# Kernel tuning notes

Hardware: AMD Instinct MI355X
Metric: run time of the kernel (lower is better)

Reference implementation:

```python
import jax, jax.numpy as jnp
import numpy as np

# --- Cl(3,0,1) projective geometric algebra structure constants (GATr blade order) ---
BLADES = [(), (0,), (1,), (2,), (3,), (0, 1), (0, 2), (0, 3), (1, 2), (1, 3), (2, 3),
          (0, 1, 2), (0, 1, 3), (0, 2, 3), (1, 2, 3), (0, 1, 2, 3)]
IDX = {b: i for i, b in enumerate(BLADES)}
METRIC = [0.0, 1.0, 1.0, 1.0]  # e0 degenerate, e1,e2,e3 square to +1


def _mul_blades(a, b):
    """Multiply two basis blades; returns (sign, sorted_blade_tuple)."""
    lst = list(a) + list(b)
    sign = 1.0
    changed = True
    while changed:
        changed = False
        k = 0
        while k < len(lst) - 1:
            if lst[k] > lst[k + 1]:
                lst[k], lst[k + 1] = lst[k + 1], lst[k]
                sign = -sign
                changed = True
            elif lst[k] == lst[k + 1]:
                sign *= METRIC[lst[k]]
                del lst[k:k + 2]
                changed = True
            else:
                k += 1
    return sign, tuple(lst)


def _tables():
    gp = np.zeros((16, 16, 16), np.float32)
    outer = np.zeros((16, 16, 16), np.float32)
    for j, bj in enumerate(BLADES):
        for k, bk in enumerate(BLADES):
            s, bl = _mul_blades(bj, bk)
            if s != 0.0:
                gp[IDX[bl], j, k] = s
            if set(bj).isdisjoint(bk):  # outer product: nonzero only for disjoint blades
                outer[IDX[bl], j, k] = s
    # dual map D: blade -> signed complement, with blade ^ complement = sign * e0123
    D = np.zeros((16, 16), np.float32)
    for j, bj in enumerate(BLADES):
        comp = tuple(i for i in range(4) if i not in bj)
        s, _ = _mul_blades(bj, comp)
        D[IDX[comp], j] = s
    # join(x, y) = dual(dual(x) ^ dual(y))  ->  bilinear tensor [16,16,16]
    join = np.einsum('ai,ijk,jb,kc->abc', D, outer, D, D).astype(np.float32)
    # Pin-equivariant linear basis: 5 grade projections + 4 e0-wedge-per-grade maps
    grades = np.array([len(b) for b in BLADES])
    basis = np.zeros((9, 16, 16), np.float32)
    for g in range(5):
        basis[g] = np.diag((grades == g).astype(np.float32))
    e0_mul = outer[:, IDX[(0,)], :]  # x -> e0 ^ x
    for g in range(4):
        basis[5 + g] = e0_mul * (grades == g)[None, :].astype(np.float32)
    return gp, join, basis


B, N = 8, 4096
IN_MV, HID, OUT_MV = 32, 32, 32
HALF = HID // 2
IN_S, OUT_S = 64, 64
NB = 9


def setup_inputs() -> dict:
    key = jax.random.key(0)
    ks = jax.random.split(key, 16)
    gp, jn, basis = _tables()

    def wmv(k, o, i):
        return jax.random.normal(k, (o, i, NB), jnp.float32) / np.sqrt(i * NB)

    def ws(k, o, i):
        return jax.random.normal(k, (o, i), jnp.float32) / np.sqrt(i)

    return dict(
        multivectors=jax.random.normal(ks[0], (B, N, IN_MV, 16), jnp.float32),
        reference_mv=jax.random.normal(ks[1], (B, N, 16), jnp.float32),
        scalars=jax.random.normal(ks[2], (B, N, IN_S), jnp.float32),
        basis=jnp.asarray(basis), gp=jnp.asarray(gp), jn=jnp.asarray(jn),
        w_left_mv=wmv(ks[3], HALF, IN_MV), w_left_s=ws(ks[4], HALF, IN_S),
        w_right_mv=wmv(ks[5], HALF, IN_MV), w_right_s=ws(ks[6], HALF, IN_S),
        w_jl_mv=wmv(ks[7], HALF, IN_MV), w_jl_s=ws(ks[8], HALF, IN_S),
        w_jr_mv=wmv(ks[9], HALF, IN_MV), w_jr_s=ws(ks[10], HALF, IN_S),
        w_out_mv=wmv(ks[11], OUT_MV, HID), w_out_s2mv=ws(ks[12], OUT_MV, IN_S),
        w_out_mvs2s=ws(ks[13], OUT_S, HID), w_out_s2s=ws(ks[14], OUT_S, IN_S),
    )


def _equi_linear(x, s, w_mv, w_s, basis):
    # fold the 9 equivariant basis maps into the channel-mixing weight once (tiny)
    W = jnp.einsum('oib,bjk->oijk', w_mv, basis)  # [out, in, 16, 16]
    out = jnp.einsum('oijk,...ik->...oj', W, x)   # (..., out, 16)
    # scalar inputs feed the multivector scalar component (blade index 0)
    out = out.at[..., 0].add(jnp.einsum('os,...s->...o', w_s, s))
    return out


def reference(multivectors, reference_mv, scalars, basis, gp, jn,
              w_left_mv, w_left_s, w_right_mv, w_right_s, w_jl_mv, w_jl_s,
              w_jr_mv, w_jr_s, w_out_mv, w_out_s2mv, w_out_mvs2s, w_out_s2s):
    left = _equi_linear(multivectors, scalars, w_left_mv, w_left_s, basis)
    right = _equi_linear(multivectors, scalars, w_right_mv, w_right_s, basis)
    gp_out = jnp.einsum('ijk,...cj,...ck->...ci', gp, left, right)  # geometric product

    jl = _equi_linear(multivectors, scalars, w_jl_mv, w_jl_s, basis)
    jr = _equi_linear(multivectors, scalars, w_jr_mv, w_jr_s, basis)
    # equivariant join, scaled by pseudoscalar (e0123) component of the reference
    join_out = jnp.einsum('ijk,...cj,...ck->...ci', jn, jl, jr) * reference_mv[..., None, 15:16]

    hidden = jnp.concatenate([gp_out, join_out], axis=-2)  # (..., HID, 16)
    out_mv = _equi_linear(hidden, scalars, w_out_mv, w_out_s2mv, basis)
    out_s = jnp.einsum('oc,...c->...o', w_out_mvs2s, hidden[..., 0]) \
        + jnp.einsum('os,...s->...o', w_out_s2s, scalars)
    return out_mv, out_s
```

## Files before the change

kernel.cpp:

```cpp
#include <hip/hip_runtime.h>
#include <stdint.h>


#define NPOS_TOTAL 32768

typedef __attribute__((ext_vector_type(8))) short short8;
typedef __attribute__((ext_vector_type(4))) float f32x4;
#define MFMA16(a,b,c) __builtin_amdgcn_mfma_f32_16x16x32_bf16((a),(b),(c),0,0,0)

constexpr int BLADE_MASK[16] = {0,1,2,4,8,3,5,9,6,10,12,7,11,13,14,15};
constexpr int MASK2IDX[16]   = {0,1,2,5,3,6,8,11,4,7,9,12,10,13,14,15};

struct MulRes { int sign; int mask; };

constexpr MulRes mul_blades(int ma, int mb) {
  int lst[8] = {0,0,0,0,0,0,0,0};
  int n = 0;
  for (int g = 0; g < 4; ++g) if ((ma >> g) & 1) lst[n++] = g;
  for (int g = 0; g < 4; ++g) if ((mb >> g) & 1) lst[n++] = g;
  int sign = 1;
  bool changed = true;
  while (changed) {
    changed = false;
    int k = 0;
    while (k + 1 < n) {
      if (lst[k] > lst[k+1]) {
        int t = lst[k]; lst[k] = lst[k+1]; lst[k+1] = t;
        sign = -sign; changed = true;
      } else if (lst[k] == lst[k+1]) {
        if (lst[k] == 0) sign = 0;
        for (int m = k; m + 2 < n; ++m) lst[m] = lst[m+2];
        n -= 2; changed = true;
      } else {
        ++k;
      }
    }
  }
  int mask = 0;
  for (int m = 0; m < n; ++m) mask |= (1 << lst[m]);
  if (sign == 0) mask = 0;
  return MulRes{sign, mask};
}

struct Tables {
  float gp_sgn[16][16]; int gp_idx[16][16];
  float jn_sgn[16][16]; int jn_idx[16][16];
  constexpr Tables() : gp_sgn{}, gp_idx{}, jn_sgn{}, jn_idx{} {
    for (int j = 0; j < 16; ++j) {
      for (int k = 0; k < 16; ++k) {
        MulRes r = mul_blades(BLADE_MASK[j], BLADE_MASK[k]);
        gp_sgn[j][k] = (float)r.sign;
        gp_idx[j][k] = MASK2IDX[r.mask & 15];
        jn_sgn[j][k] = 0.0f; jn_idx[j][k] = 0;
        int mb = BLADE_MASK[j], mc = BLADE_MASK[k];
        if ((mb | mc) == 15) {
          int cb = 15 ^ mb, cc = 15 ^ mc;
          MulRes sb = mul_blades(mb, cb);
          MulRes sc = mul_blades(mc, cc);
          MulRes ro = mul_blades(cb, cc);
          int imask = ro.mask;
          int amask = 15 ^ imask;
          MulRes si = mul_blades(imask, amask);
          jn_sgn[j][k] = (float)(si.sign * ro.sign * sb.sign * sc.sign);
          jn_idx[j][k] = MASK2IDX[amask & 15];
        }
      }
    }
  }
};
constexpr Tables TBL{};

constexpr int GRADE[16] = {0,1,1,1,1,2,2,2,2,2,2,3,3,3,3,4};
constexpr int E0_TGT[8]  = {1,5,6,7,11,12,13,15};
constexpr int E0_SRC[8]  = {0,2,3,4,8,9,10,14};
constexpr int E0_SLOT[8] = {5,6,6,6,7,7,7,8};

__device__ __forceinline__ float bflo(unsigned u) { return __uint_as_float(u << 16); }
__device__ __forceinline__ float bfhi(unsigned u) { return __uint_as_float(u & 0xffff0000u); }
__device__ __forceinline__ unsigned pk2(float a, float b) {
  unsigned ua = __float_as_uint(a), ub = __float_as_uint(b);
  unsigned ra = (ua + 0x7fffu + ((ua >> 16) & 1u)) >> 16;
  unsigned rb = (ub + 0x7fffu + ((ub >> 16) & 1u)) >> 16;
  return (ra & 0xffffu) | ((rb & 0xffffu) << 16);
}
__device__ __forceinline__ unsigned short bf1(float a) {
  unsigned ua = __float_as_uint(a);
  return (unsigned short)((ua + 0x7fffu + ((ua >> 16) & 1u)) >> 16);
}

__global__ void gb_prep(const float* __restrict__ wlmv, const float* __restrict__ wrmv,
                        const float* __restrict__ wjlmv, const float* __restrict__ wjrmv,
                        const float* __restrict__ wls,  const float* __restrict__ wrs,
                        const float* __restrict__ wjls, const float* __restrict__ wjrs,
                        const float* __restrict__ womv, const float* __restrict__ ws2mv,
                        const float* __restrict__ wm2s, const float* __restrict__ ws2s,
                        uint4* __restrict__ wpk) {
  int t = blockIdx.x * 256 + threadIdx.x;
  if (t >= 78 * 64) return;
  int blk = t >> 6, l = t & 63;
  int m = l & 15, q = l >> 4;
  float v[8];
  if (blk < 36) {
    int slot = blk >> 2, ot = blk & 3;
    const float* wmv[4] = {wlmv, wrmv, wjlmv, wjrmv};
    for (int jj = 0; jj < 8; ++jj) {
      int k = q * 8 + jj;
      v[jj] = wmv[ot][m * 288 + k * 9 + slot];
    }
  } else if (blk < 44) {
    int b = blk - 36, h = b >> 2, ot = b & 3;
    const float* wsc[4] = {wls, wrs, wjls, wjrs};
    for (int jj = 0; jj < 8; ++jj) {
      int k = q * 8 + jj;
      v[jj] = wsc[ot][m * 64 + h * 32 + k];
    }
  } else if (blk < 62) {
    int b = blk - 44, slot = b >> 1, ot = b & 1;
    int o = ot * 16 + m;
    for (int jj = 0; jj < 8; ++jj) {
      int k = q * 8 + jj;
      v[jj] = womv[o * 288 + k * 9 + slot];
    }
  } else if (blk < 66) {
    int b = blk - 62, h = b >> 1, ot = b & 1;
    int o = ot * 16 + m;
    for (int jj = 0; jj < 8; ++jj) {
      int k = q * 8 + jj;
      v[jj] = ws2mv[o * 64 + h * 32 + k];
    }
  } else if (blk < 70) {
    int ot = blk - 66, o = ot * 16 + m;
    for (int jj = 0; jj < 8; ++jj) {
      int k = q * 8 + jj;
      v[jj] = wm2s[o * 32 + k];
    }
  } else {
    int b = blk - 70, half = b >> 2, ot = b & 3;
    int o = ot * 16 + m;
    for (int jj = 0; jj < 8; ++jj) {
      int k = q * 8 + jj;
      v[jj] = ws2s[o * 64 + half * 32 + k];
    }
  }
  uint4 u;
  u.x = pk2(v[0], v[1]); u.y = pk2(v[2], v[3]);
  u.z = pk2(v[4], v[5]); u.w = pk2(v[6], v[7]);
  wpk[t] = u;
}

__global__ __launch_bounds__(256, 2) void gb_main(
    const float* __restrict__ mv, const float* __restrict__ ref,
    const float* __restrict__ s, const uint4* __restrict__ wpk,
    float* __restrict__ out_mv, float* __restrict__ out_s) {
  __shared__ __align__(16) char smem[54016];
  unsigned short* xs_e = (unsigned short*)smem;
  unsigned*       xs_w = (unsigned*)smem;
  unsigned short* hl_e = (unsigned short*)smem;
  unsigned*       yl_w = (unsigned*)(smem + 16640);

  const int tid  = threadIdx.x;
  const int wave = tid >> 6, lane = tid & 63;
  const int lm = lane & 15, lq = lane >> 4;
  const int P0 = blockIdx.x * 16;

  short8 wg[5];
  #pragma unroll
  for (int g = 0; g < 5; ++g)
    wg[g] = __builtin_bit_cast(short8, wpk[(g * 4 + wave) * 64 + lane]);

  const float rs = ref[((size_t)(P0 + (tid & 15))) * 16 + 15];

  const float4* mv4 = (const float4*)mv + (size_t)P0 * 128;
  #pragma unroll
  for (int kk = 0; kk < 4; ++kk) {
    int e = tid + kk * 256;
    int p = e >> 6, sub = e & 63, i2 = sub >> 2, jg = sub & 3;
    float4 fa = mv4[p * 128 + i2 * 8 + jg];
    float4 fb = mv4[p * 128 + i2 * 8 + 4 + jg];
    int base = p * 260 + jg * 4 * 16 + i2;
    xs_w[base + 0 * 16] = pk2(fa.x, fb.x);
    xs_w[base + 1 * 16] = pk2(fa.y, fb.y);
    xs_w[base + 2 * 16] = pk2(fa.z, fb.z);
    xs_w[base + 3 * 16] = pk2(fa.w, fb.w);
  }

  short8 sfrag[2];
  {
    const float4* s4 = (const float4*)s + ((size_t)(P0 + lm)) * 16;
    #pragma unroll
    for (int h = 0; h < 2; ++h) {
      float4 a = s4[h * 8 + lq * 2];
      float4 b = s4[h * 8 + lq * 2 + 1];
      uint4 u;
      u.x = pk2(a.x, a.y); u.y = pk2(a.z, a.w);
      u.z = pk2(b.x, b.y); u.w = pk2(b.z, b.w);
      sfrag[h] = __builtin_bit_cast(short8, u);
    }
  }
  __syncthreads();

  {
    short8 bx[16];
    #pragma unroll
    for (int c = 0; c < 16; ++c)
      bx[c] = *(const short8*)&xs_e[lm * 520 + c * 32 + lq * 8];
    short8 we[4];
    #pragma unroll
    for (int sidx = 0; sidx < 4; ++sidx)
      we[sidx] = __builtin_bit_cast(short8, wpk[((5 + sidx) * 4 + wave) * 64 + lane]);
    short8 wsc1[2];
    #pragma unroll
    for (int h = 0; h < 2; ++h)
      wsc1[h] = __builtin_bit_cast(short8, wpk[(36 + h * 4 + wave) * 64 + lane]);

    f32x4 zf = {0.f, 0.f, 0.f, 0.f};
    f32x4 acc[16];
    #pragma unroll
    for (int j = 0; j < 16; ++j) acc[j] = zf;
    #pragma unroll
    for (int j = 0; j < 16; ++j)
      acc[j] = MFMA16(wg[GRADE[j]], bx[j], acc[j]);
    #pragma unroll
    for (int m = 0; m < 8; ++m)
      acc[E0_TGT[m]] = MFMA16(we[E0_SLOT[m] - 5], bx[E0_SRC[m]], acc[E0_TGT[m]]);
    #pragma unroll
    for (int h = 0; h < 2; ++h)
      acc[0] = MFMA16(wsc1[h], sfrag[h], acc[0]);
    #pragma unroll
    for (int jp = 0; jp < 8; ++jp) {
      #pragma unroll
      for (int r = 0; r < 4; ++r) {
        int o = wave * 16 + lq * 4 + r;
        yl_w[o * 146 + lm * 9 + jp] = pk2(acc[2 * jp][r], acc[2 * jp + 1][r]);
      }
    }
  }
  __syncthreads();

  {
    const int pos = tid & 15;
    const int hc  = tid >> 4;
    float L[16], R[16], H[16];
    {
      const unsigned* pL = yl_w + hc * 146 + pos * 9;
      const unsigned* pR = yl_w + (16 + hc) * 146 + pos * 9;
      #pragma unroll
      for (int q = 0; q < 8; ++q) {
        unsigned a = pL[q], b = pR[q];
        L[2*q] = bflo(a); L[2*q+1] = bfhi(a);
        R[2*q] = bflo(b); R[2*q+1] = bfhi(b);
      }
    }
    #pragma unroll
    for (int q = 0; q < 16; ++q) H[q] = 0.f;
    #pragma unroll
    for (int j = 0; j < 16; ++j)
      #pragma unroll
      for (int k = 0; k < 16; ++k)
        if (TBL.gp_sgn[j][k] != 0.0f)
          H[TBL.gp_idx[j][k]] += TBL.gp_sgn[j][k] * L[j] * R[k];
    #pragma unroll
    for (int j = 0; j < 16; ++j)
      hl_e[pos * 520 + j * 32 + hc] = bf1(H[j]);
    {
      const unsigned* pJ = yl_w + (32 + hc) * 146 + pos * 9;
      const unsigned* pK = yl_w + (48 + hc) * 146 + pos * 9;
      #pragma unroll
      for (int q = 0; q < 8; ++q) {
        unsigned a = pJ[q];
        L[2*q] = bflo(a) * rs; L[2*q+1] = bfhi(a) * rs;
      }
      #pragma unroll
      for (int q = 0; q < 8; ++q) {
        unsigned a = pK[q];
        R[2*q] = bflo(a); R[2*q+1] = bfhi(a);
      }
    }
    #pragma unroll
    for (int q = 0; q < 16; ++q) H[q] = 0.f;
    #pragma unroll
    for (int j = 0; j < 16; ++j)
      #pragma unroll
      for (int k = 0; k < 16; ++k)
        if (TBL.jn_sgn[j][k] != 0.0f)
          H[TBL.jn_idx[j][k]] += TBL.jn_sgn[j][k] * L[j] * R[k];
    #pragma unroll
    for (int j = 0; j < 16; ++j)
      hl_e[pos * 520 + j * 32 + 16 + hc] = bf1(H[j]);
  }

  short8 w3[11];
  if (wave < 2) {
    #pragma unroll
    for (int g = 0; g < 9; ++g)
      w3[g] = __builtin_bit_cast(short8, wpk[(44 + g * 2 + wave) * 64 + lane]);
    #pragma unroll
    for (int h = 0; h < 2; ++h)
      w3[9 + h] = __builtin_bit_cast(short8, wpk[(62 + h * 2 + wave) * 64 + lane]);
  } else {
    int w2 = wave - 2;
    #pragma unroll
    for (int t2 = 0; t2 < 2; ++t2) {
      int otg = w2 * 2 + t2;
      w3[t2 * 3 + 0] = __builtin_bit_cast(short8, wpk[(66 + otg) * 64 + lane]);
      w3[t2 * 3 + 1] = __builtin_bit_cast(short8, wpk[(70 + otg) * 64 + lane]);
      w3[t2 * 3 + 2] = __builtin_bit_cast(short8, wpk[(74 + otg) * 64 + lane]);
    }
  }
  __syncthreads();

  if (wave < 2) {
    short8 bh[16];
    #pragma unroll
    for (int j = 0; j < 16; ++j)
      bh[j] = *(const short8*)&hl_e[lm * 520 + j * 32 + lq * 8];
    f32x4 zf = {0.f, 0.f, 0.f, 0.f};
    f32x4 a3[16];
    #pragma unroll
    for (int j = 0; j < 16; ++j) a3[j] = zf;
    #pragma unroll
    for (int j = 0; j < 16; ++j)
      a3[j] = MFMA16(w3[GRADE[j]], bh[j], a3[j]);
    #pragma unroll
    for (int m = 0; m < 8; ++m)
      a3[E0_TGT[m]] = MFMA16(w3[E0_SLOT[m]], bh[E0_SRC[m]], a3[E0_TGT[m]]);
    #pragma unroll
    for (int h = 0; h < 2; ++h)
      a3[0] = MFMA16(w3[9 + h], sfrag[h], a3[0]);
    float* ob = out_mv + ((size_t)(P0 + lm)) * 512 + (size_t)(wave * 16 + lq * 4) * 16;
    #pragma unroll
    for (int r = 0; r < 4; ++r) {
      #pragma unroll
      for (int g = 0; g < 4; ++g) {
        *(float4*)(ob + r * 16 + g * 4) =
            make_float4(a3[4*g][r], a3[4*g+1][r], a3[4*g+2][r], a3[4*g+3][r]);
      }
    }
  } else {
    short8 bh0 = *(const short8*)&hl_e[lm * 520 + lq * 8];
    f32x4 zf = {0.f, 0.f, 0.f, 0.f};
    #pragma unroll
    for (int t2 = 0; t2 < 2; ++t2) {
      int otg = (wave - 2) * 2 + t2;
      f32x4 aS = zf;
      aS = MFMA16(w3[t2 * 3 + 0], bh0, aS);
      aS = MFMA16(w3[t2 * 3 + 1], sfrag[0], aS);
      aS = MFMA16(w3[t2 * 3 + 2], sfrag[1], aS);
      float* osb = out_s + ((size_t)(P0 + lm)) * 64 + otg * 16 + lq * 4;
      *(float4*)osb = make_float4(aS[0], aS[1], aS[2], aS[3]);
    }
  }
}

extern "C" void kernel_launch(void* const* d_in, const int* in_sizes, int n_in,
                              void* d_out, int out_size, void* d_ws, size_t ws_size,
                              hipStream_t stream) {
  (void)in_sizes; (void)n_in; (void)out_size; (void)ws_size;
  const float* mv    = (const float*)d_in[0];
  const float* ref   = (const float*)d_in[1];
  const float* s     = (const float*)d_in[2];
  const float* wlmv  = (const float*)d_in[6];
  const float* wls   = (const float*)d_in[7];
  const float* wrmv  = (const float*)d_in[8];
  const float* wrs   = (const float*)d_in[9];
  const float* wjlmv = (const float*)d_in[10];
  const float* wjls  = (const float*)d_in[11];
  const float* wjrmv = (const float*)d_in[12];
  const float* wjrs  = (const float*)d_in[13];
  const float* womv  = (const float*)d_in[14];
  const float* ws2mv = (const float*)d_in[15];
  const float* wm2s  = (const float*)d_in[16];
  const float* ws2s  = (const float*)d_in[17];

  float* out_mv = (float*)d_out;
  float* out_s  = out_mv + (size_t)NPOS_TOTAL * 32 * 16;
  uint4* wpk = (uint4*)d_ws;

  gb_prep<<<20, 256, 0, stream>>>(wlmv, wrmv, wjlmv, wjrmv, wls, wrs, wjls, wjrs,
                                  womv, ws2mv, wm2s, ws2s, wpk);
  gb_main<<<NPOS_TOTAL / 16, 256, 0, stream>>>(mv, ref, s, wpk, out_mv, out_s);
}
```

Baseline: 186.1 us.

## Process four position tiles per block with software-pipelined prefetch and LDS-resident weights

After: 195.7 us. 5.2% more time.

```diff
diff --git a/kernel.cpp b/kernel.cpp
--- a/kernel.cpp
+++ b/kernel.cpp
@@ -3,6 +3,13 @@
 
 
 #define NPOS_TOTAL 32768
+#define T_TILES 4
+
+#define WLDS_FRAGS 78
+#define XS_SZ      20736
+#define XS0_OFF    79872
+#define YL_OFF     121344
+#define SMEM_BYTES 158720
 
 typedef __attribute__((ext_vector_type(8))) short short8;
 typedef __attribute__((ext_vector_type(4))) float f32x4;
@@ -148,207 +155,222 @@
   wpk[t] = u;
 }
 
-__global__ __launch_bounds__(256, 2) void gb_main(
+__global__ __launch_bounds__(256, 1) void gb_main(
     const float* __restrict__ mv, const float* __restrict__ ref,
     const float* __restrict__ s, const uint4* __restrict__ wpk,
     float* __restrict__ out_mv, float* __restrict__ out_s) {
-  __shared__ __align__(16) char smem[54016];
-  unsigned short* xs_e = (unsigned short*)smem;
-  unsigned*       xs_w = (unsigned*)smem;
-  unsigned short* hl_e = (unsigned short*)smem;
-  unsigned*       yl_w = (unsigned*)(smem + 16640);
+  __shared__ __align__(16) char smem[SMEM_BYTES];
+  unsigned* ylw = (unsigned*)(smem + YL_OFF);
 
   const int tid  = threadIdx.x;
   const int wave = tid >> 6, lane = tid & 63;
   const int lm = lane & 15, lq = lane >> 4;
-  const int P0 = blockIdx.x * 16;
-
-  short8 wg[5];
-  #pragma unroll
-  for (int g = 0; g < 5; ++g)
-    wg[g] = __builtin_bit_cast(short8, wpk[(g * 4 + wave) * 64 + lane]);
-
-  const float rs = ref[((size_t)(P0 + (tid & 15))) * 16 + 15];
-
-  const float4* mv4 = (const float4*)mv + (size_t)P0 * 128;
-  #pragma unroll
-  for (int kk = 0; kk < 4; ++kk) {
-    int e = tid + kk * 256;
-    int p = e >> 6, sub = e & 63, i2 = sub >> 2, jg = sub & 3;
-    float4 fa = mv4[p * 128 + i2 * 8 + jg];
-    float4 fb = mv4[p * 128 + i2 * 8 + 4 + jg];
-    int base = p * 260 + jg * 4 * 16 + i2;
-    xs_w[base + 0 * 16] = pk2(fa.x, fb.x);
-    xs_w[base + 1 * 16] = pk2(fa.y, fb.y);
-    xs_w[base + 2 * 16] = pk2(fa.z, fb.z);
-    xs_w[base + 3 * 16] = pk2(fa.w, fb.w);
+  const int i2v = lane >> 2, jg = lane & 3;
+  const int P0b = blockIdx.x * (T_TILES * 16);
+
+  {
+    const uint4* src = wpk;
+    uint4* dst = (uint4*)smem;
+    for (int i = tid; i < WLDS_FRAGS * 64; i += 256) dst[i] = src[i];
   }
 
-  short8 sfrag[2];
-  {
-    const float4* s4 = (const float4*)s + ((size_t)(P0 + lm)) * 16;
-    #pragma unroll
-    for (int h = 0; h < 2; ++h) {
-      float4 a = s4[h * 8 + lq * 2];
-      float4 b = s4[h * 8 + lq * 2 + 1];
+  auto frag = [&](int f) -> short8 {
+    return *(const short8*)(smem + ((size_t)(f * 64 + lane)) * 16);
+  };
+
+  float4 mvp[8];
+  float4 sp[4];
+  short8 sprev[2], scur[2];
+  sprev[0] = short8{}; sprev[1] = short8{};
+  scur[0] = short8{}; scur[1] = short8{};
+  float rs_cur = 0.f, rs_next = 0.f;
+
+  #pragma unroll 1
+  for (int t = -1; t <= T_TILES; ++t) {
+    if (t + 1 < T_TILES) {
+      const int P0n = P0b + (t + 1) * 16;
+      const float4* mv4n = (const float4*)mv + (size_t)P0n * 128;
+      #pragma unroll
+      for (int kk = 0; kk < 4; ++kk) {
+        int p = wave + kk * 4;
+        mvp[2 * kk]     = mv4n[p * 128 + i2v * 8 + jg];
+        mvp[2 * kk + 1] = mv4n[p * 128 + i2v * 8 + 4 + jg];
+      }
+      const float4* s4n = (const float4*)s + ((size_t)(P0n + lm)) * 16;
+      sp[0] = s4n[lq * 2];     sp[1] = s4n[lq * 2 + 1];
+      sp[2] = s4n[8 + lq * 2]; sp[3] = s4n[8 + lq * 2 + 1];
+      rs_next = ref[((size_t)(P0n + (tid >> 4))) * 16 + 15];
+    }
+
+    if (t > 0) {
+      const unsigned short* hb =
+          (const unsigned short*)(smem + XS0_OFF + ((t - 1) & 1) * XS_SZ);
+      const int P0p = P0b + (t - 1) * 16;
+      if (wave < 2) {
+        short8 w3g[5], w3e[4], w3s[2];
+        #pragma unroll
+        for (int g = 0; g < 5; ++g) w3g[g] = frag(44 + g * 2 + wave);
+        #pragma unroll
+        for (int m = 0; m < 4; ++m) w3e[m] = frag(44 + (5 + m) * 2 + wave);
+        #pragma unroll
+        for (int h = 0; h < 2; ++h) w3s[h] = frag(62 + h * 2 + wave);
+        short8 bh[16];
+        #pragma unroll
+        for (int j = 0; j < 16; ++j)
+          bh[j] = *(const short8*)&hb[lm * 520 + j * 32 + lq * 8];
+        f32x4 zf = {0.f, 0.f, 0.f, 0.f};
+        f32x4 a3[16];
+        #pragma unroll
+        for (int j = 0; j < 16; ++j) a3[j] = zf;
+        #pragma unroll
+        for (int j = 0; j < 16; ++j)
+          a3[j] = MFMA16(w3g[GRADE[j]], bh[j], a3[j]);
+        #pragma unroll
+        for (int m = 0; m < 8; ++m)
+          a3[E0_TGT[m]] = MFMA16(w3e[E0_SLOT[m] - 5], bh[E0_SRC[m]], a3[E0_TGT[m]]);
+        #pragma unroll
+        for (int h = 0; h < 2; ++h)
+          a3[0] = MFMA16(w3s[h], sprev[h], a3[0]);
+        float* ob = out_mv + ((size_t)(P0p + lm)) * 512 + (size_t)(wave * 16 + lq * 4) * 16;
+        #pragma unroll
+        for (int r = 0; r < 4; ++r) {
+          #pragma unroll
+          for (int g = 0; g < 4; ++g) {
+            *(float4*)(ob + r * 16 + g * 4) =
+                make_float4(a3[4 * g][r], a3[4 * g + 1][r], a3[4 * g + 2][r], a3[4 * g + 3][r]);
+          }
+        }
+      } else {
+        short8 bh0 = *(const short8*)&hb[lm * 520 + lq * 8];
+        f32x4 zf = {0.f, 0.f, 0.f, 0.f};
+        #pragma unroll
+        for (int t2 = 0; t2 < 2; ++t2) {
+          int otg = (wave - 2) * 2 + t2;
+          f32x4 aS = zf;
+          aS = MFMA16(frag(66 + otg), bh0, aS);
+          aS = MFMA16(frag(70 + otg), sprev[0], aS);
+          aS = MFMA16(frag(74 + otg), sprev[1], aS);
+          float* osb = out_s + ((size_t)(P0p + lm)) * 64 + otg * 16 + lq * 4;
+          *(float4*)osb = make_float4(aS[0], aS[1], aS[2], aS[3]);
+        }
+      }
+    }
+
+    if ((unsigned)t < (unsigned)T_TILES) {
+      const unsigned short* xe =
+          (const unsigned short*)(smem + XS0_OFF + (t & 1) * XS_SZ);
+      short8 wg[5], we[4], wsc[2];
+      #pragma unroll
+      for (int g = 0; g < 5; ++g) wg[g] = frag(g * 4 + wave);
+      #pragma unroll
+      for (int m = 0; m < 4; ++m) we[m] = frag((5 + m) * 4 + wave);
+      #pragma unroll
+      for (int h = 0; h < 2; ++h) wsc[h] = frag(36 + h * 4 + wave);
+      short8 bx[16];
+      #pragma unroll
+      for (int c = 0; c < 16; ++c)
+        bx[c] = *(const short8*)&xe[lm * 648 + c * 40 + lq * 8];
+      f32x4 zf = {0.f, 0.f, 0.f, 0.f};
+      f32x4 acc[16];
+      #pragma unroll
+      for (int j = 0; j < 16; ++j) acc[j] = zf;
+      #pragma unroll
+      for (int j = 0; j < 16; ++j)
+        acc[j] = MFMA16(wg[GRADE[j]], bx[j], acc[j]);
+      #pragma unroll
+      for (int m = 0; m < 8; ++m)
+        acc[E0_TGT[m]] = MFMA16(we[E0_SLOT[m] - 5], bx[E0_SRC[m]], acc[E0_TGT[m]]);
+      #pragma unroll
+      for (int h = 0; h < 2; ++h)
+        acc[0] = MFMA16(wsc[h], scur[h], acc[0]);
+      #pragma unroll
+      for (int jp = 0; jp < 8; ++jp) {
+        #pragma unroll
+        for (int r = 0; r < 4; ++r) {
+          int o = wave * 16 + lq * 4 + r;
+          ylw[o * 146 + lm * 9 + jp] = pk2(acc[2 * jp][r], acc[2 * jp + 1][r]);
+        }
+      }
+    }
+    __syncthreads();
+
+    if ((unsigned)t < (unsigned)T_TILES) {
+      const int pos = tid >> 4;
+      const int hc  = tid & 15;
+      unsigned short* hl = (unsigned short*)(smem + XS0_OFF + (t & 1) * XS_SZ);
+      float L[16], R[16], H[16];
+      {
+        const unsigned* pL = ylw + hc * 146 + pos * 9;
+        const unsigned* pR = ylw + (16 + hc) * 146 + pos * 9;
+        #pragma unroll
+        for (int q = 0; q < 8; ++q) {
+          unsigned a = pL[q], b = pR[q];
+          L[2 * q] = bflo(a); L[2 * q + 1] = bfhi(a);
+          R[2 * q] = bflo(b); R[2 * q + 1] = bfhi(b);
+        }
+      }
+      #pragma unroll
+      for (int q = 0; q < 16; ++q) H[q] = 0.f;
+      #pragma unroll
+      for (int j = 0; j < 16; ++j)
+        #pragma unroll
+        for (int k = 0; k < 16; ++k)
+          if (TBL.gp_sgn[j][k] != 0.0f)
+            H[TBL.gp_idx[j][k]] += TBL.gp_sgn[j][k] * L[j] * R[k];
+      #pragma unroll
+      for (int j = 0; j < 16; ++j)
+        hl[pos * 520 + j * 32 + hc] = bf1(H[j]);
+      {
+        const unsigned* pJ = ylw + (32 + hc) * 146 + pos * 9;
+        const unsigned* pK = ylw + (48 + hc) * 146 + pos * 9;
+        #pragma unroll
+        for (int q = 0; q < 8; ++q) {
+          unsigned a = pJ[q];
+          L[2 * q] = bflo(a) * rs_cur; L[2 * q + 1] = bfhi(a) * rs_cur;
+        }
+        #pragma unroll
+        for (int q = 0; q < 8; ++q) {
+          unsigned a = pK[q];
+          R[2 * q] = bflo(a); R[2 * q + 1] = bfhi(a);
+        }
+      }
+      #pragma unroll
+      for (int q = 0; q < 16; ++q) H[q] = 0.f;
+      #pragma unroll
+      for (int j = 0; j < 16; ++j)
+        #pragma unroll
+        for (int k = 0; k < 16; ++k)
+          if (TBL.jn_sgn[j][k] != 0.0f)
+            H[TBL.jn_idx[j][k]] += TBL.jn_sgn[j][k] * L[j] * R[k];
+      #pragma unroll
+      for (int j = 0; j < 16; ++j)
+        hl[pos * 520 + j * 32 + 16 + hc] = bf1(H[j]);
+    }
+
+    sprev[0] = scur[0]; sprev[1] = scur[1];
+
+    if (t + 1 < T_TILES) {
+      unsigned* xw = (unsigned*)(smem + XS0_OFF + ((t + 1) & 1) * XS_SZ);
+      #pragma unroll
+      for (int kk = 0; kk < 4; ++kk) {
+        int p = wave + kk * 4;
+        int base = p * 324 + jg * 80 + i2v;
+        float4 fa = mvp[2 * kk], fb = mvp[2 * kk + 1];
+        xw[base + 0 * 20] = pk2(fa.x, fb.x);
+        xw[base + 1 * 20] = pk2(fa.y, fb.y);
+        xw[base + 2 * 20] = pk2(fa.z, fb.z);
+        xw[base + 3 * 20] = pk2(fa.w, fb.w);
+      }
       uint4 u;
-      u.x = pk2(a.x, a.y); u.y = pk2(a.z, a.w);
-      u.z = pk2(b.x, b.y); u.w = pk2(b.z, b.w);
-      sfrag[h] = __builtin_bit_cast(short8, u);
-    }
-  }
-  __syncthreads();
-
-  {
-    short8 bx[16];
-    #pragma unroll
-    for (int c = 0; c < 16; ++c)
-      bx[c] = *(const short8*)&xs_e[lm * 520 + c * 32 + lq * 8];
-    short8 we[4];
-    #pragma unroll
-    for (int sidx = 0; sidx < 4; ++sidx)
-      we[sidx] = __builtin_bit_cast(short8, wpk[((5 + sidx) * 4 + wave) * 64 + lane]);
-    short8 wsc1[2];
-    #pragma unroll
-    for (int h = 0; h < 2; ++h)
-      wsc1[h] = __builtin_bit_cast(short8, wpk[(36 + h * 4 + wave) * 64 + lane]);
-
-    f32x4 zf = {0.f, 0.f, 0.f, 0.f};
-    f32x4 acc[16];
-    #pragma unroll
-    for (int j = 0; j < 16; ++j) acc[j] = zf;
-    #pragma unroll
-    for (int j = 0; j < 16; ++j)
-      acc[j] = MFMA16(wg[GRADE[j]], bx[j], acc[j]);
-    #pragma unroll
-    for (int m = 0; m < 8; ++m)
-      acc[E0_TGT[m]] = MFMA16(we[E0_SLOT[m] - 5], bx[E0_SRC[m]], acc[E0_TGT[m]]);
-    #pragma unroll
-    for (int h = 0; h < 2; ++h)
-      acc[0] = MFMA16(wsc1[h], sfrag[h], acc[0]);
-    #pragma unroll
-    for (int jp = 0; jp < 8; ++jp) {
-      #pragma unroll
-      for (int r = 0; r < 4; ++r) {
-        int o = wave * 16 + lq * 4 + r;
-        yl_w[o * 146 + lm * 9 + jp] = pk2(acc[2 * jp][r], acc[2 * jp + 1][r]);
-      }
-    }
-  }
-  __syncthreads();
-
-  {
-    const int pos = tid & 15;
-    const int hc  = tid >> 4;
-    float L[16], R[16], H[16];
-    {
-      const unsigned* pL = yl_w + hc * 146 + pos * 9;
-      const unsigned* pR = yl_w + (16 + hc) * 146 + pos * 9;
-      #pragma unroll
-      for (int q = 0; q < 8; ++q) {
-        unsigned a = pL[q], b = pR[q];
-        L[2*q] = bflo(a); L[2*q+1] = bfhi(a);
-        R[2*q] = bflo(b); R[2*q+1] = bfhi(b);
-      }
-    }
-    #pragma unroll
-    for (int q = 0; q < 16; ++q) H[q] = 0.f;
-    #pragma unroll
-    for (int j = 0; j < 16; ++j)
-      #pragma unroll
-      for (int k = 0; k < 16; ++k)
-        if (TBL.gp_sgn[j][k] != 0.0f)
-          H[TBL.gp_idx[j][k]] += TBL.gp_sgn[j][k] * L[j] * R[k];
-    #pragma unroll
-    for (int j = 0; j < 16; ++j)
-      hl_e[pos * 520 + j * 32 + hc] = bf1(H[j]);
-    {
-      const unsigned* pJ = yl_w + (32 + hc) * 146 + pos * 9;
-      const unsigned* pK = yl_w + (48 + hc) * 146 + pos * 9;
-      #pragma unroll
-      for (int q = 0; q < 8; ++q) {
-        unsigned a = pJ[q];
-        L[2*q] = bflo(a) * rs; L[2*q+1] = bfhi(a) * rs;
-      }
-      #pragma unroll
-      for (int q = 0; q < 8; ++q) {
-        unsigned a = pK[q];
-        R[2*q] = bflo(a); R[2*q+1] = bfhi(a);
-      }
-    }
-    #pragma unroll
-    for (int q = 0; q < 16; ++q) H[q] = 0.f;
-    #pragma unroll
-    for (int j = 0; j < 16; ++j)
-      #pragma unroll
-      for (int k = 0; k < 16; ++k)
-        if (TBL.jn_sgn[j][k] != 0.0f)
-          H[TBL.jn_idx[j][k]] += TBL.jn_sgn[j][k] * L[j] * R[k];
-    #pragma unroll
-    for (int j = 0; j < 16; ++j)
-      hl_e[pos * 520 + j * 32 + 16 + hc] = bf1(H[j]);
-  }
-
-  short8 w3[11];
-  if (wave < 2) {
-    #pragma unroll
-    for (int g = 0; g < 9; ++g)
-      w3[g] = __builtin_bit_cast(short8, wpk[(44 + g * 2 + wave) * 64 + lane]);
-    #pragma unroll
-    for (int h = 0; h < 2; ++h)
-      w3[9 + h] = __builtin_bit_cast(short8, wpk[(62 + h * 2 + wave) * 64 + lane]);
-  } else {
-    int w2 = wave - 2;
-    #pragma unroll
-    for (int t2 = 0; t2 < 2; ++t2) {
-      int otg = w2 * 2 + t2;
-      w3[t2 * 3 + 0] = __builtin_bit_cast(short8, wpk[(66 + otg) * 64 + lane]);
-      w3[t2 * 3 + 1] = __builtin_bit_cast(short8, wpk[(70 + otg) * 64 + lane]);
-      w3[t2 * 3 + 2] = __builtin_bit_cast(short8, wpk[(74 + otg) * 64 + lane]);
-    }
-  }
-  __syncthreads();
-
-  if (wave < 2) {
-    short8 bh[16];
-    #pragma unroll
-    for (int j = 0; j < 16; ++j)
-      bh[j] = *(const short8*)&hl_e[lm * 520 + j * 32 + lq * 8];
-    f32x4 zf = {0.f, 0.f, 0.f, 0.f};
-    f32x4 a3[16];
-    #pragma unroll
-    for (int j = 0; j < 16; ++j) a3[j] = zf;
-    #pragma unroll
-    for (int j = 0; j < 16; ++j)
-      a3[j] = MFMA16(w3[GRADE[j]], bh[j], a3[j]);
-    #pragma unroll
-    for (int m = 0; m < 8; ++m)
-      a3[E0_TGT[m]] = MFMA16(w3[E0_SLOT[m]], bh[E0_SRC[m]], a3[E0_TGT[m]]);
-    #pragma unroll
-    for (int h = 0; h < 2; ++h)
-      a3[0] = MFMA16(w3[9 + h], sfrag[h], a3[0]);
-    float* ob = out_mv + ((size_t)(P0 + lm)) * 512 + (size_t)(wave * 16 + lq * 4) * 16;
-    #pragma unroll
-    for (int r = 0; r < 4; ++r) {
-      #pragma unroll
-      for (int g = 0; g < 4; ++g) {
-        *(float4*)(ob + r * 16 + g * 4) =
-            make_float4(a3[4*g][r], a3[4*g+1][r], a3[4*g+2][r], a3[4*g+3][r]);
-      }
-    }
-  } else {
-    short8 bh0 = *(const short8*)&hl_e[lm * 520 + lq * 8];
-    f32x4 zf = {0.f, 0.f, 0.f, 0.f};
-    #pragma unroll
-    for (int t2 = 0; t2 < 2; ++t2) {
-      int otg = (wave - 2) * 2 + t2;
-      f32x4 aS = zf;
-      aS = MFMA16(w3[t2 * 3 + 0], bh0, aS);
-      aS = MFMA16(w3[t2 * 3 + 1], sfrag[0], aS);
-      aS = MFMA16(w3[t2 * 3 + 2], sfrag[1], aS);
-      float* osb = out_s + ((size_t)(P0 + lm)) * 64 + otg * 16 + lq * 4;
-      *(float4*)osb = make_float4(aS[0], aS[1], aS[2], aS[3]);
-    }
+      u.x = pk2(sp[0].x, sp[0].y); u.y = pk2(sp[0].z, sp[0].w);
+      u.z = pk2(sp[1].x, sp[1].y); u.w = pk2(sp[1].z, sp[1].w);
+      scur[0] = __builtin_bit_cast(short8, u);
+      u.x = pk2(sp[2].x, sp[2].y); u.y = pk2(sp[2].z, sp[2].w);
+      u.z = pk2(sp[3].x, sp[3].y); u.w = pk2(sp[3].z, sp[3].w);
+      scur[1] = __builtin_bit_cast(short8, u);
+      rs_cur = rs_next;
+    }
+    __syncthreads();
   }
 }
 
@@ -378,5 +400,5 @@
 
   gb_prep<<<20, 256, 0, stream>>>(wlmv, wrmv, wjlmv, wjrmv, wls, wrs, wjls, wjrs,
                                   womv, ws2mv, wm2s, ws2s, wpk);
-  gb_main<<<NPOS_TOTAL / 16, 256, 0, stream>>>(mv, ref, s, wpk, out_mv, out_s);
-}
+  gb_main<<<NPOS_TOTAL / (T_TILES * 16), 256, 0, stream>>>(mv, ref, s, wpk, out_mv, out_s);
+}
```

## Stage multivector input via direct global-to-LDS loads with swizzle, hoist weight loads

Applied to the files above, without the earlier changes.

Measured after the change: 184.7 us. About the same (-0.8%).

```diff
diff --git a/kernel.cpp b/kernel.cpp
--- a/kernel.cpp
+++ b/kernel.cpp
@@ -3,6 +3,8 @@
 
 
 #define NPOS_TOTAL 32768
+#define M_OFF   16640
+#define SMEM_BYTES 54016
 
 typedef __attribute__((ext_vector_type(8))) short short8;
 typedef __attribute__((ext_vector_type(4))) float f32x4;
@@ -88,6 +90,10 @@
   return (unsigned short)((ua + 0x7fffu + ((ua >> 16) & 1u)) >> 16);
 }
 
+__device__ __forceinline__ int cswz(int c) {
+  return (c & ~7) | ((c ^ (c >> 3)) & 7);
+}
+
 __global__ void gb_prep(const float* __restrict__ wlmv, const float* __restrict__ wrmv,
                         const float* __restrict__ wjlmv, const float* __restrict__ wjrmv,
                         const float* __restrict__ wls,  const float* __restrict__ wrs,
@@ -152,49 +158,74 @@
     const float* __restrict__ mv, const float* __restrict__ ref,
     const float* __restrict__ s, const uint4* __restrict__ wpk,
     float* __restrict__ out_mv, float* __restrict__ out_s) {
-  __shared__ __align__(16) char smem[54016];
+  __shared__ __align__(16) char smem[SMEM_BYTES];
   unsigned short* xs_e = (unsigned short*)smem;
   unsigned*       xs_w = (unsigned*)smem;
   unsigned short* hl_e = (unsigned short*)smem;
-  unsigned*       yl_w = (unsigned*)(smem + 16640);
+  unsigned*       yl_w = (unsigned*)(smem + M_OFF);
 
   const int tid  = threadIdx.x;
   const int wave = tid >> 6, lane = tid & 63;
   const int lm = lane & 15, lq = lane >> 4;
   const int P0 = blockIdx.x * 16;
 
-  short8 wg[5];
+  short8 wg[5], we[4], wsc1[2];
   #pragma unroll
   for (int g = 0; g < 5; ++g)
     wg[g] = __builtin_bit_cast(short8, wpk[(g * 4 + wave) * 64 + lane]);
-
-  const float rs = ref[((size_t)(P0 + (tid & 15))) * 16 + 15];
-
-  const float4* mv4 = (const float4*)mv + (size_t)P0 * 128;
   #pragma unroll
-  for (int kk = 0; kk < 4; ++kk) {
-    int e = tid + kk * 256;
-    int p = e >> 6, sub = e & 63, i2 = sub >> 2, jg = sub & 3;
-    float4 fa = mv4[p * 128 + i2 * 8 + jg];
-    float4 fb = mv4[p * 128 + i2 * 8 + 4 + jg];
-    int base = p * 260 + jg * 4 * 16 + i2;
-    xs_w[base + 0 * 16] = pk2(fa.x, fb.x);
-    xs_w[base + 1 * 16] = pk2(fa.y, fb.y);
-    xs_w[base + 2 * 16] = pk2(fa.z, fb.z);
-    xs_w[base + 3 * 16] = pk2(fa.w, fb.w);
-  }
+  for (int m = 0; m < 4; ++m)
+    we[m] = __builtin_bit_cast(short8, wpk[((5 + m) * 4 + wave) * 64 + lane]);
+  #pragma unroll
+  for (int h = 0; h < 2; ++h)
+    wsc1[h] = __builtin_bit_cast(short8, wpk[(36 + h * 4 + wave) * 64 + lane]);
+  const float rs = ref[((size_t)(P0 + (tid >> 4))) * 16 + 15];
+  float4 sp[4];
+  {
+    const float4* s4 = (const float4*)s + ((size_t)(P0 + lm)) * 16;
+    sp[0] = s4[lq * 2];     sp[1] = s4[lq * 2 + 1];
+    sp[2] = s4[8 + lq * 2]; sp[3] = s4[8 + lq * 2 + 1];
+  }
+  {
+    const char* mvb = (const char*)mv + (size_t)P0 * 2048;
+    const int sl = cswz(lane);
+    #pragma unroll
+    for (int i = 0; i < 8; ++i) {
+      int window = wave * 8 + i;
+      __builtin_amdgcn_global_load_lds(
+          (const __attribute__((address_space(1))) unsigned int*)(mvb + (size_t)(window * 64 + sl) * 16),
+          (__attribute__((address_space(3))) unsigned int*)(smem + M_OFF + window * 1024),
+          16, 0, 0);
+    }
+  }
+  __builtin_amdgcn_sched_barrier(0);
+  __syncthreads();
 
   short8 sfrag[2];
   {
-    const float4* s4 = (const float4*)s + ((size_t)(P0 + lm)) * 16;
-    #pragma unroll
-    for (int h = 0; h < 2; ++h) {
-      float4 a = s4[h * 8 + lq * 2];
-      float4 b = s4[h * 8 + lq * 2 + 1];
-      uint4 u;
-      u.x = pk2(a.x, a.y); u.y = pk2(a.z, a.w);
-      u.z = pk2(b.x, b.y); u.w = pk2(b.z, b.w);
-      sfrag[h] = __builtin_bit_cast(short8, u);
+    uint4 u;
+    u.x = pk2(sp[0].x, sp[0].y); u.y = pk2(sp[0].z, sp[0].w);
+    u.z = pk2(sp[1].x, sp[1].y); u.w = pk2(sp[1].z, sp[1].w);
+    sfrag[0] = __builtin_bit_cast(short8, u);
+    u.x = pk2(sp[2].x, sp[2].y); u.y = pk2(sp[2].z, sp[2].w);
+    u.z = pk2(sp[3].x, sp[3].y); u.w = pk2(sp[3].z, sp[3].w);
+    sfrag[1] = __builtin_bit_cast(short8, u);
+  }
+
+  {
+    const float4* M4 = (const float4*)(smem + M_OFF);
+    const int i2 = lane >> 2, jg = lane & 3;
+    #pragma unroll
+    for (int kk = 0; kk < 4; ++kk) {
+      int p = kk * 4 + wave;
+      int cfa = p * 128 + i2 * 8 + jg;
+      float4 fa = M4[cswz(cfa)];
+      float4 fb = M4[cswz(cfa + 4)];
+      int base = p * 260 + jg * 64 + i2;
+      xs_w[base + 0]  = pk2(fa.x, fb.x);
+      xs_w[base + 16] = pk2(fa.y, fb.y);
+      xs_w[base + 32] = pk2(fa.z, fb.z);
+      xs_w[base + 48] = pk2(fa.w, fb.w);
     }
   }
   __syncthreads();
@@ -204,15 +235,6 @@
     #pragma unroll
     for (int c = 0; c < 16; ++c)
       bx[c] = *(const short8*)&xs_e[lm * 520 + c * 32 + lq * 8];
-    short8 we[4];
-    #pragma unroll
-    for (int sidx = 0; sidx < 4; ++sidx)
-      we[sidx] = __builtin_bit_cast(short8, wpk[((5 + sidx) * 4 + wave) * 64 + lane]);
-    short8 wsc1[2];
-    #pragma unroll
-    for (int h = 0; h < 2; ++h)
-      wsc1[h] = __builtin_bit_cast(short8, wpk[(36 + h * 4 + wave) * 64 + lane]);
-
     f32x4 zf = {0.f, 0.f, 0.f, 0.f};
     f32x4 acc[16];
     #pragma unroll
@@ -238,8 +260,8 @@
   __syncthreads();
 
   {
-    const int pos = tid & 15;
-    const int hc  = tid >> 4;
+    const int pos = tid >> 4;
+    const int hc  = tid & 15;
     float L[16], R[16], H[16];
     {
       const unsigned* pL = yl_w + hc * 146 + pos * 9;
@@ -307,6 +329,7 @@
       w3[t2 * 3 + 2] = __builtin_bit_cast(short8, wpk[(74 + otg) * 64 + lane]);
     }
   }
+  __builtin_amdgcn_sched_barrier(0);
   __syncthreads();
 
   if (wave < 2) {
```
